# Optimization experiments

Measured on AMD Instinct MI355X. Metric: run time of the kernel, lower is better.

The kernel has to match this reference:

```python
import jax, jax.numpy as jnp
import numpy as np

NUM_CLASSES = 10

def setup_inputs() -> dict:
    key = jax.random.key(0)
    k1, k2, k3 = jax.random.split(key, 3)
    X = jax.random.normal(k1, (1024, 128), dtype=jnp.float32)
    X_train = jax.random.normal(k2, (100000, 128), dtype=jnp.float32)
    y_train = jax.random.randint(k3, (100000,), 0, NUM_CLASSES, dtype=jnp.int64)
    return {"X": X, "X_train": X_train, "y_train": y_train, "k": 5}


def reference(X, X_train, y_train, k):
    test_sq = jnp.sum(X * X, axis=1, keepdims=True)            # [T, 1]
    train_sq = jnp.sum(X_train * X_train, axis=1)[None, :]     # [1, N]
    cross = X @ X_train.T                                      # [T, N]
    dists = jnp.sqrt(jnp.maximum(test_sq + train_sq - 2.0 * cross, 0.0))
    # top-k nearest: smallest distances == largest negated distances
    _, idx = jax.lax.top_k(-dists, k)                          # [T, k]
    labels = y_train[idx]                                      # [T, k]
    # majority vote; argmax returns the smallest label on ties,
    # matching most_frq_smaller semantics
    counts = jnp.sum(jax.nn.one_hot(labels, NUM_CLASSES, dtype=jnp.int32), axis=1)  # [T, C]
    y_pred = jnp.argmax(counts, axis=1).astype(jnp.float32)    # torch.zeros default float
    return y_pred
```

## Files before the change

kernel.cpp:

```cpp
#include <hip/hip_runtime.h>
#include <cfloat>
#include <cstdint>


#define NTRAIN 100000
#define D 128
#define T 1024
#define TB 128
#define NT 32
#define KNN 5
#define NUM_CLASSES 10
#define NCH 125
#define NTILE_TOT 3125
#define TILE_HALVES 8192

typedef _Float16 half8 __attribute__((ext_vector_type(8)));
typedef float f32x16 __attribute__((ext_vector_type(16)));

#define MFMA(a, b, c) __builtin_amdgcn_mfma_f32_32x32x16_f16((a), (b), (c), 0, 0, 0)

struct Cand { float s; int j; };

__device__ __forceinline__ bool better(float s, int j, const Cand& c) {
    return (s > c.s) || (s == c.s && j < c.j);
}

__device__ __forceinline__ void ins5(Cand t5[KNN], float s, int j) {
    if (!better(s, j, t5[4])) return;
    if (better(s, j, t5[0]))      { t5[4]=t5[3]; t5[3]=t5[2]; t5[2]=t5[1]; t5[1]=t5[0]; t5[0]={s,j}; }
    else if (better(s, j, t5[1])) { t5[4]=t5[3]; t5[3]=t5[2]; t5[2]=t5[1]; t5[1]={s,j}; }
    else if (better(s, j, t5[2])) { t5[4]=t5[3]; t5[3]=t5[2]; t5[2]={s,j}; }
    else if (better(s, j, t5[3])) { t5[4]=t5[3]; t5[3]={s,j}; }
    else                          { t5[4]={s,j}; }
}

__device__ __forceinline__ void gload_lds16(const void* g, void* l) {
    __builtin_amdgcn_global_load_lds(
        (const __attribute__((address_space(1))) uint32_t*)g,
        (__attribute__((address_space(3))) uint32_t*)l, 16, 0, 0);
}

__global__ __launch_bounds__(256)
void knn_norms(const float* __restrict__ XT, uint32_t* __restrict__ nrmp) {
    const int j = blockIdx.x * 256 + threadIdx.x;
    if (j >= NTRAIN) return;
    const float4* row = (const float4*)&XT[(size_t)j * D];
    float p[32];
#pragma unroll
    for (int c = 0; c < 32; ++c) {
        float4 v = row[c];
        p[c] = v.x * v.x + v.y * v.y + v.z * v.z + v.w * v.w;
    }
#pragma unroll
    for (int s = 1; s < 32; s <<= 1)
#pragma unroll
        for (int i = 0; i < 32; i += 2 * s) p[i] += p[i + s];
    const float m = -0.5f * p[0];
    const _Float16 mh = (_Float16)m;
    const _Float16 ml = (_Float16)(m - (float)mh);
    union { _Float16 h[2]; uint32_t u; } cv;
    cv.h[0] = mh; cv.h[1] = ml;
    nrmp[j] = cv.u;
}

__global__ __launch_bounds__(256)
void knn_pack(const float* __restrict__ XT, _Float16* __restrict__ XTs,
              uint32_t* __restrict__ nrmp) {
    __shared__ __align__(16) float sb[32 * D];
    const int tid  = threadIdx.x;
    const int tile = blockIdx.x;
    const float4* src = (const float4*)&XT[(size_t)tile * 32 * D];
#pragma unroll
    for (int p = 0; p < 4; ++p)
        *(float4*)&sb[(p * 256 + tid) * 4] = src[p * 256 + tid];
    __syncthreads();

    {
        const int ks = tid >> 5, kh = (tid >> 4) & 1, rp = (tid & 15) * 2;
        const int c0 = ks * 16 + kh * 8;
        _Float16* outp = &XTs[(size_t)tile * TILE_HALVES + tid * 16];
#pragma unroll
        for (int rr = 0; rr < 2; ++rr) {
            const float* s = &sb[(rp + rr) * D + c0];
            half8 hv, lv;
#pragma unroll
            for (int e = 0; e < 8; ++e) {
                float v = s[e];
                _Float16 hh = (_Float16)v;
                hv[e] = hh; lv[e] = (_Float16)(v - (float)hh);
            }
            *(half8*)&outp[rr * 8]        = hv;
            *(half8*)&outp[4096 + rr * 8] = lv;
        }
    }
    {
        const int row = tid >> 3, seg = tid & 7;
        const float4* rp4 = (const float4*)&sb[row * D];
        float q[4];
#pragma unroll
        for (int c = 0; c < 4; ++c) {
            float4 v = rp4[seg * 4 + c];
            q[c] = v.x * v.x + v.y * v.y + v.z * v.z + v.w * v.w;
        }
        float part = (q[0] + q[1]) + (q[2] + q[3]);
        part += __shfl_xor(part, 1);
        part += __shfl_xor(part, 2);
        part += __shfl_xor(part, 4);
        if (seg == 0) {
            const float m = -0.5f * part;
            const _Float16 mh = (_Float16)m;
            const _Float16 ml = (_Float16)(m - (float)mh);
            union { _Float16 h[2]; uint32_t u; } cv;
            cv.h[0] = mh; cv.h[1] = ml;
            nrmp[tile * 32 + row] = cv.u;
        }
    }
}

template <bool SPLIT>
__global__ __launch_bounds__(256, 3)
void knn_mfma(const float* __restrict__ X, const float* __restrict__ XT,
              const _Float16* __restrict__ XTs, const uint32_t* __restrict__ nrmp,
              Cand* __restrict__ part, int nch, int chunk) {
    __shared__ __align__(16) _Float16 lds[2][TILE_HALVES];

    const int tid  = threadIdx.x;
    const int lane = tid & 63;
    const int wv   = tid >> 6;
    const int bx   = blockIdx.x;
    const int bc   = blockIdx.y;

    half8 Bh[8], Bl[8];
    {
        const int trow = bx * TB + wv * 32 + (lane & 31);
        const float* xp = &X[(size_t)trow * D + (lane >> 5) * 8];
#pragma unroll
        for (int ks = 0; ks < 8; ++ks) {
            float4 v0 = *(const float4*)&xp[ks * 16];
            float4 v1 = *(const float4*)&xp[ks * 16 + 4];
            float a[8] = {v0.x, v0.y, v0.z, v0.w, v1.x, v1.y, v1.z, v1.w};
#pragma unroll
            for (int e = 0; e < 8; ++e) {
                _Float16 hh = (_Float16)a[e];
                Bh[ks][e] = hh;
                Bl[ks][e] = (_Float16)(a[e] - (float)hh);
            }
        }
    }
    half8 B8;
#pragma unroll
    for (int e = 0; e < 8; ++e) B8[e] = (_Float16)0.0f;
    if (lane < 32) B8[0] = (_Float16)1.0f;

    const int srow = tid & 31;
    const int ksp  = tid >> 5;
    float a16[16];

    auto issue_stage_split = [&](int buf, int tile) {
        const _Float16* g = &XTs[(size_t)tile * TILE_HALVES + wv * 512 + lane * 8];
        _Float16* l = &lds[buf][wv * 512];
#pragma unroll
        for (int p = 0; p < 4; ++p)
            gload_lds16(g + p * 2048, l + p * 2048);
    };
    auto issue_loads = [&](int jb) {
        int j = jb + srow;
        if (j > NTRAIN - 1) j = NTRAIN - 1;
        const float4* p = (const float4*)&XT[(size_t)j * D + ksp * 16];
        float4 v0 = p[0], v1 = p[1], v2 = p[2], v3 = p[3];
        a16[0]=v0.x; a16[1]=v0.y; a16[2]=v0.z; a16[3]=v0.w;
        a16[4]=v1.x; a16[5]=v1.y; a16[6]=v1.z; a16[7]=v1.w;
        a16[8]=v2.x; a16[9]=v2.y; a16[10]=v2.z; a16[11]=v2.w;
        a16[12]=v3.x; a16[13]=v3.y; a16[14]=v3.z; a16[15]=v3.w;
    };
    auto write_stage = [&](int buf) {
        half8 hv0, lv0, hv1, lv1;
#pragma unroll
        for (int e = 0; e < 8; ++e) {
            _Float16 hh = (_Float16)a16[e];
            hv0[e] = hh; lv0[e] = (_Float16)(a16[e] - (float)hh);
        }
#pragma unroll
        for (int e = 0; e < 8; ++e) {
            _Float16 hh = (_Float16)a16[8 + e];
            hv1[e] = hh; lv1[e] = (_Float16)(a16[8 + e] - (float)hh);
        }
        _Float16* base = &lds[buf][ksp * 512 + srow * 8];
        *(half8*)(base)              = hv0;
        *(half8*)(base + 256)        = hv1;
        *(half8*)(base + 4096)       = lv0;
        *(half8*)(base + 4096 + 256) = lv1;
    };

    Cand top5[KNN];
#pragma unroll
    for (int e = 0; e < KNN; ++e) top5[e] = {-FLT_MAX, 0x7fffffff};

    const int jc0 = bc * chunk;
    const int ntiles = chunk >> 5;
    const int tile0 = jc0 >> 5;

    if (SPLIT) {
        issue_stage_split(0, tile0);
    } else {
        issue_loads(jc0);
        write_stage(0);
    }
    __syncthreads();

    for (int t = 0; t < ntiles; ++t) {
        const int jb = jc0 + t * NT;
        if (!SPLIT && jb >= NTRAIN) break;
        const int buf = t & 1;
        const bool more = (t + 1 < ntiles);

        if (SPLIT) {
            if (more) issue_stage_split(buf ^ 1, tile0 + t + 1);
        } else {
            if (more) issue_loads(jb + NT);
        }

        int nj = jb + (lane & 31);
        if (!SPLIT && nj > NTRAIN - 1) nj = NTRAIN - 1;
        uint32_t nv = nrmp[nj];
        if (lane >= 32) nv = 0;

        f32x16 acc;
#pragma unroll
        for (int e = 0; e < 16; ++e) acc[e] = 0.f;

        const _Float16* rbase = &lds[buf][lane * 8];
        __builtin_amdgcn_s_setprio(1);
#pragma unroll
        for (int ks = 0; ks < 8; ++ks) {
            half8 ah = *(const half8*)(rbase + ks * 512);
            half8 al = *(const half8*)(rbase + 4096 + ks * 512);
            acc = MFMA(ah, Bh[ks], acc);
            acc = MFMA(ah, Bl[ks], acc);
            acc = MFMA(al, Bh[ks], acc);
        }
        {
            union { uint32_t u; _Float16 h[2]; } cv; cv.u = nv;
            half8 augh, augl;
#pragma unroll
            for (int e = 0; e < 8; ++e) { augh[e] = (_Float16)0.0f; augl[e] = (_Float16)0.0f; }
            augh[0] = cv.h[0];
            augl[0] = cv.h[1];
            acc = MFMA(augh, B8, acc);
            acc = MFMA(augl, B8, acc);
        }
        __builtin_amdgcn_s_setprio(0);

        if (!SPLIT && more) write_stage(buf ^ 1);

        const int rb = 4 * (lane >> 5);
        float qm[4];
#pragma unroll
        for (int qq = 0; qq < 4; ++qq)
            qm[qq] = fmaxf(fmaxf(acc[qq * 4], acc[qq * 4 + 1]),
                           fmaxf(acc[qq * 4 + 2], acc[qq * 4 + 3]));
        const float M = fmaxf(fmaxf(qm[0], qm[1]), fmaxf(qm[2], qm[3]));
        if (M > top5[4].s) {
#pragma unroll
            for (int qq = 0; qq < 4; ++qq) {
                if (qm[qq] > top5[4].s) {
#pragma unroll
                    for (int r = 0; r < 4; ++r) {
                        const int reg = qq * 4 + r;
                        const float s = acc[reg];
                        if (s > top5[4].s) {
                            const int j = jb + (reg & 3) + 8 * (reg >> 2) + rb;
                            if (SPLIT || j < NTRAIN) ins5(top5, s, j);
                        }
                    }
                }
            }
        }
        __syncthreads();
    }

    {
        float os[KNN]; int oj[KNN];
#pragma unroll
        for (int e = 0; e < KNN; ++e) {
            os[e] = __shfl_xor(top5[e].s, 32);
            oj[e] = __shfl_xor(top5[e].j, 32);
        }
#pragma unroll
        for (int e = 0; e < KNN; ++e) ins5(top5, os[e], oj[e]);
        if (lane < 32) {
            const int test = bx * TB + wv * 32 + lane;
            Cand* pp = &part[((size_t)test * nch + bc) * KNN];
#pragma unroll
            for (int e = 0; e < KNN; ++e) pp[e] = top5[e];
        }
    }
}

__global__ __launch_bounds__(256)
void knn_vote2(const Cand* __restrict__ part, const int* __restrict__ y,
               float* __restrict__ out, int nch) {
    const int tid  = threadIdx.x;
    const int lane = tid & 63;
    const int test = blockIdx.x * 4 + (tid >> 6);
    if (test >= T) return;

    Cand best[KNN];
#pragma unroll
    for (int e = 0; e < KNN; ++e) best[e] = {-FLT_MAX, 0x7fffffff};

    for (int c = lane; c < nch; c += 64) {
        const Cand* pp = &part[((size_t)test * nch + c) * KNN];
#pragma unroll
        for (int e = 0; e < KNN; ++e) {
            const Cand cc = pp[e];
            if ((unsigned)cc.j < (unsigned)NTRAIN) ins5(best, cc.s, cc.j);
        }
    }
#pragma unroll
    for (int off = 32; off >= 1; off >>= 1) {
        float os[KNN]; int oj[KNN];
#pragma unroll
        for (int e = 0; e < KNN; ++e) {
            os[e] = __shfl_xor(best[e].s, off);
            oj[e] = __shfl_xor(best[e].j, off);
        }
#pragma unroll
        for (int e = 0; e < KNN; ++e)
            if ((unsigned)oj[e] < (unsigned)NTRAIN) ins5(best, os[e], oj[e]);
    }
    if (lane == 0) {
        int lbl[KNN];
#pragma unroll
        for (int e = 0; e < KNN; ++e) lbl[e] = y[best[e].j];
        int bestc = 0, bestcnt = -1;
#pragma unroll
        for (int c = 0; c < NUM_CLASSES; ++c) {
            int cnt = 0;
#pragma unroll
            for (int e = 0; e < KNN; ++e) cnt += (lbl[e] == c) ? 1 : 0;
            if (cnt > bestcnt) { bestcnt = cnt; bestc = c; }
        }
        out[test] = (float)bestc;
    }
}

extern "C" void kernel_launch(void* const* d_in, const int* in_sizes, int n_in,
                              void* d_out, int out_size, void* d_ws, size_t ws_size,
                              hipStream_t stream) {
    const float* X  = (const float*)d_in[0];
    const float* XT = (const float*)d_in[1];
    const int*   y  = (const int*)d_in[2];

    const size_t xts_bytes = (size_t)NTILE_TOT * TILE_HALVES * 2;
    const size_t nrm_bytes = ((size_t)NTRAIN * 4 + 255) & ~(size_t)255;
    const size_t per_chunk = (size_t)T * KNN * sizeof(Cand);
    const size_t base = xts_bytes + nrm_bytes;

    if (ws_size >= base + NCH * per_chunk) {
        _Float16* XTs  = (_Float16*)d_ws;
        uint32_t* nrmp = (uint32_t*)((char*)d_ws + xts_bytes);
        Cand*     part = (Cand*)((char*)d_ws + base);
        const int chunk = NTRAIN / NCH;
        knn_pack<<<NTILE_TOT, 256, 0, stream>>>(XT, XTs, nrmp);
        knn_mfma<true><<<dim3(T / TB, NCH), 256, 0, stream>>>(X, XT, XTs, nrmp, part, NCH, chunk);
        knn_vote2<<<T / 4, 256, 0, stream>>>(part, y, (float*)d_out, NCH);
    } else {
        uint32_t* nrmp = (uint32_t*)d_ws;
        Cand*     part = (Cand*)((char*)d_ws + nrm_bytes);
        int fch = NCH;
        if (nrm_bytes + (size_t)fch * per_chunk > ws_size) {
            size_t avail = (ws_size > nrm_bytes) ? (ws_size - nrm_bytes) : 0;
            fch = (int)(avail / per_chunk);
            if (fch < 1) fch = 1;
        }
        const int chunk = (((NTRAIN + fch - 1) / fch) + (NT - 1)) & ~(NT - 1);
        knn_norms<<<(NTRAIN + 255) / 256, 256, 0, stream>>>(XT, nrmp);
        knn_mfma<false><<<dim3(T / TB, fch), 256, 0, stream>>>(X, XT, nullptr, nrmp, part, fch, chunk);
        knn_vote2<<<T / 4, 256, 0, stream>>>(part, y, (float*)d_out, fch);
    }
}
```

Baseline: 177.9 us.

## Seed per-test top-k threshold from a sampled prepass and raise occupancy

A prepass runs the MFMA distance kernel over 8 chunks and stores each chunk's 5th-best score per test row. The main pass starts each thread's top-5 list at the maximum of those scores, so candidate insertions beyond the pruning bound are skipped. The change also raises launch bounds from 3 to 4 waves per SIMD and moves the barrier ahead of the selection step. It replaces the hierarchical max pre-check with a flat per-register compare and walks the global load pointer incrementally. The costs are an extra kernel launch and a small amount of duplicated GEMM work, plus possible register pressure from the tighter occupancy target.

```diff
diff --git a/kernel.cpp b/kernel.cpp
--- a/kernel.cpp
+++ b/kernel.cpp
@@ -11,6 +11,8 @@
 #define KNN 5
 #define NUM_CLASSES 10
 #define NCH 125
+#define CHUNK 800
+#define NSAMP 8
 #define NTILE_TOT 3125
 #define TILE_HALVES 8192
 
@@ -117,11 +119,12 @@
     }
 }
 
-template <bool SPLIT>
-__global__ __launch_bounds__(256, 3)
+template <bool SPLIT, bool THRESH>
+__global__ __launch_bounds__(256, 4)
 void knn_mfma(const float* __restrict__ X, const float* __restrict__ XT,
               const _Float16* __restrict__ XTs, const uint32_t* __restrict__ nrmp,
-              Cand* __restrict__ part, int nch, int chunk) {
+              Cand* __restrict__ part, int nch, int chunk,
+              const float* __restrict__ thrb, float* __restrict__ thrw) {
     __shared__ __align__(16) _Float16 lds[2][TILE_HALVES];
 
     const int tid  = threadIdx.x;
@@ -152,13 +155,19 @@
     for (int e = 0; e < 8; ++e) B8[e] = (_Float16)0.0f;
     if (lane < 32) B8[0] = (_Float16)1.0f;
 
+    f32x16 kZero;
+#pragma unroll
+    for (int e = 0; e < 16; ++e) kZero[e] = 0.f;
+
     const int srow = tid & 31;
     const int ksp  = tid >> 5;
     float a16[16];
 
-    auto issue_stage_split = [&](int buf, int tile) {
-        const _Float16* g = &XTs[(size_t)tile * TILE_HALVES + wv * 512 + lane * 8];
-        _Float16* l = &lds[buf][wv * 512];
+    _Float16* const l0 = &lds[0][wv * 512];
+    _Float16* const l1 = &lds[1][wv * 512];
+
+    auto issue_stage_split = [&](int buf, const _Float16* g) {
+        _Float16* l = buf ? l1 : l0;
 #pragma unroll
         for (int p = 0; p < 4; ++p)
             gload_lds16(g + p * 2048, l + p * 2048);
@@ -192,16 +201,24 @@
         *(half8*)(base + 4096 + 256) = lv1;
     };
 
+    float s0 = -FLT_MAX;
+    if (!THRESH && thrb != nullptr) {
+        const int col = bx * TB + wv * 32 + (lane & 31);
+#pragma unroll
+        for (int c = 0; c < NSAMP; ++c) s0 = fmaxf(s0, thrb[c * T + col]);
+    }
     Cand top5[KNN];
 #pragma unroll
-    for (int e = 0; e < KNN; ++e) top5[e] = {-FLT_MAX, 0x7fffffff};
+    for (int e = 0; e < KNN; ++e) top5[e] = {s0, 0x7fffffff};
 
     const int jc0 = bc * chunk;
     const int ntiles = chunk >> 5;
     const int tile0 = jc0 >> 5;
 
+    const _Float16* gcur = &XTs[(size_t)tile0 * TILE_HALVES + wv * 512 + lane * 8];
+
     if (SPLIT) {
-        issue_stage_split(0, tile0);
+        issue_stage_split(0, gcur);
     } else {
         issue_loads(jc0);
         write_stage(0);
@@ -215,7 +232,8 @@
         const bool more = (t + 1 < ntiles);
 
         if (SPLIT) {
-            if (more) issue_stage_split(buf ^ 1, tile0 + t + 1);
+            gcur += TILE_HALVES;
+            if (more) issue_stage_split(buf ^ 1, gcur);
         } else {
             if (more) issue_loads(jb + NT);
         }
@@ -225,14 +243,18 @@
         uint32_t nv = nrmp[nj];
         if (lane >= 32) nv = 0;
 
-        f32x16 acc;
-#pragma unroll
-        for (int e = 0; e < 16; ++e) acc[e] = 0.f;
-
         const _Float16* rbase = &lds[buf][lane * 8];
         __builtin_amdgcn_s_setprio(1);
-#pragma unroll
-        for (int ks = 0; ks < 8; ++ks) {
+        f32x16 acc;
+        {
+            half8 ah = *(const half8*)(rbase);
+            half8 al = *(const half8*)(rbase + 4096);
+            acc = MFMA(ah, Bh[0], kZero);
+            acc = MFMA(ah, Bl[0], acc);
+            acc = MFMA(al, Bh[0], acc);
+        }
+#pragma unroll
+        for (int ks = 1; ks < 8; ++ks) {
             half8 ah = *(const half8*)(rbase + ks * 512);
             half8 al = *(const half8*)(rbase + 4096 + ks * 512);
             acc = MFMA(ah, Bh[ks], acc);
@@ -253,30 +275,17 @@
 
         if (!SPLIT && more) write_stage(buf ^ 1);
 
+        __syncthreads();
+
         const int rb = 4 * (lane >> 5);
-        float qm[4];
-#pragma unroll
-        for (int qq = 0; qq < 4; ++qq)
-            qm[qq] = fmaxf(fmaxf(acc[qq * 4], acc[qq * 4 + 1]),
-                           fmaxf(acc[qq * 4 + 2], acc[qq * 4 + 3]));
-        const float M = fmaxf(fmaxf(qm[0], qm[1]), fmaxf(qm[2], qm[3]));
-        if (M > top5[4].s) {
-#pragma unroll
-            for (int qq = 0; qq < 4; ++qq) {
-                if (qm[qq] > top5[4].s) {
-#pragma unroll
-                    for (int r = 0; r < 4; ++r) {
-                        const int reg = qq * 4 + r;
-                        const float s = acc[reg];
-                        if (s > top5[4].s) {
-                            const int j = jb + (reg & 3) + 8 * (reg >> 2) + rb;
-                            if (SPLIT || j < NTRAIN) ins5(top5, s, j);
-                        }
-                    }
-                }
+#pragma unroll
+        for (int reg = 0; reg < 16; ++reg) {
+            const float s = acc[reg];
+            if (s >= top5[4].s) {
+                const int j = jb + (reg & 3) + 8 * (reg >> 2) + rb;
+                if (SPLIT || j < NTRAIN) ins5(top5, s, j);
             }
         }
-        __syncthreads();
     }
 
     {
@@ -290,9 +299,13 @@
         for (int e = 0; e < KNN; ++e) ins5(top5, os[e], oj[e]);
         if (lane < 32) {
             const int test = bx * TB + wv * 32 + lane;
-            Cand* pp = &part[((size_t)test * nch + bc) * KNN];
-#pragma unroll
-            for (int e = 0; e < KNN; ++e) pp[e] = top5[e];
+            if (THRESH) {
+                thrw[bc * T + test] = top5[4].s;
+            } else {
+                Cand* pp = &part[((size_t)test * nch + bc) * KNN];
+#pragma unroll
+                for (int e = 0; e < KNN; ++e) pp[e] = top5[e];
+            }
         }
     }
 }
@@ -354,16 +367,20 @@
 
     const size_t xts_bytes = (size_t)NTILE_TOT * TILE_HALVES * 2;
     const size_t nrm_bytes = ((size_t)NTRAIN * 4 + 255) & ~(size_t)255;
+    const size_t thr_bytes = ((size_t)NSAMP * T * 4 + 255) & ~(size_t)255;
     const size_t per_chunk = (size_t)T * KNN * sizeof(Cand);
-    const size_t base = xts_bytes + nrm_bytes;
+    const size_t base = xts_bytes + nrm_bytes + thr_bytes;
 
     if (ws_size >= base + NCH * per_chunk) {
         _Float16* XTs  = (_Float16*)d_ws;
         uint32_t* nrmp = (uint32_t*)((char*)d_ws + xts_bytes);
+        float*    thr  = (float*)((char*)d_ws + xts_bytes + nrm_bytes);
         Cand*     part = (Cand*)((char*)d_ws + base);
-        const int chunk = NTRAIN / NCH;
         knn_pack<<<NTILE_TOT, 256, 0, stream>>>(XT, XTs, nrmp);
-        knn_mfma<true><<<dim3(T / TB, NCH), 256, 0, stream>>>(X, XT, XTs, nrmp, part, NCH, chunk);
+        knn_mfma<true, true><<<dim3(T / TB, NSAMP), 256, 0, stream>>>(
+            X, XT, XTs, nrmp, nullptr, NSAMP, CHUNK, nullptr, thr);
+        knn_mfma<true, false><<<dim3(T / TB, NCH), 256, 0, stream>>>(
+            X, XT, XTs, nrmp, part, NCH, CHUNK, thr, nullptr);
         knn_vote2<<<T / 4, 256, 0, stream>>>(part, y, (float*)d_out, NCH);
     } else {
         uint32_t* nrmp = (uint32_t*)d_ws;
@@ -376,7 +393,8 @@
         }
         const int chunk = (((NTRAIN + fch - 1) / fch) + (NT - 1)) & ~(NT - 1);
         knn_norms<<<(NTRAIN + 255) / 256, 256, 0, stream>>>(XT, nrmp);
-        knn_mfma<false><<<dim3(T / TB, fch), 256, 0, stream>>>(X, XT, nullptr, nrmp, part, fch, chunk);
+        knn_mfma<false, false><<<dim3(T / TB, fch), 256, 0, stream>>>(
+            X, XT, nullptr, nrmp, part, fch, chunk, nullptr, nullptr);
         knn_vote2<<<T / 4, 256, 0, stream>>>(part, y, (float*)d_out, fch);
     }
 }
```

Result: slower. 243.3 us (+36.8%).
